# Kernel tuning notes

Measured on AMD Instinct MI355X. Metric: run time of the kernel, lower is better.

## Reference

```python
import jax, jax.numpy as jnp
import numpy as np

R = 50000          # residues
P = 24             # residue_pad_length
APR = 15           # atoms per residue (<= P)
N = R * APR        # total atoms
ACD = ATD = RCD = RID = 32
N_ATOM_CODES, N_ATOM_TYPES, N_RES_CODES, MAX_SEQ = 38, 6, 21, 1024
VEC_OUT, SC_OUT = 64, 256          # irreps_out = 64x1e + 256x0e
SC_IN = P * ACD + P * ATD + RCD + RID  # 1600 scalar inputs


def setup_inputs() -> dict:
    key = jax.random.key(0)
    ks = jax.random.split(key, 10)
    return {
        "residue_base_coords": jax.random.normal(ks[0], (R, 3), jnp.float32),
        "residue_relative_coords": jax.random.normal(ks[1], (N, 3), jnp.float32),
        "residue_code_index": jax.random.randint(ks[2], (R,), 0, N_RES_CODES),
        "residue_sequence_index": jnp.arange(R) % MAX_SEQ,
        "atom_code_index": jax.random.randint(ks[3], (N,), 0, N_ATOM_CODES),
        "atom_type_index": jax.random.randint(ks[4], (N,), 0, N_ATOM_TYPES),
        "residue_index_atomwise": jnp.repeat(jnp.arange(R), APR),  # sorted, APR atoms each
        "W_atom_code": jax.random.normal(ks[5], (N_ATOM_CODES, ACD), jnp.float32),
        "W_atom_type": jax.random.normal(ks[6], (N_ATOM_TYPES, ATD), jnp.float32),
        "W_res_code": jax.random.normal(ks[7], (N_RES_CODES, RCD), jnp.float32),
        "W_res_idx": jax.random.normal(ks[8], (MAX_SEQ, RID), jnp.float32),
        "W_vec": jax.random.normal(jax.random.fold_in(key, 1), (P, VEC_OUT), jnp.float32),
        "W_sc": jax.random.normal(ks[9], (SC_IN, SC_OUT), jnp.float32),
    }


def reference(residue_base_coords, residue_relative_coords, residue_code_index,
              residue_sequence_index, atom_code_index, atom_type_index,
              residue_index_atomwise, W_atom_code, W_atom_type, W_res_code,
              W_res_idx, W_vec, W_sc):
    R_ = residue_base_coords.shape[0]
    P_ = W_vec.shape[0]
    N_ = residue_index_atomwise.shape[0]
    ri = residue_index_atomwise
    # vectorized replacement of the per-residue python loop:
    # position of each atom within its residue (residue_index_atomwise is sorted)
    offsets = jnp.searchsorted(ri, jnp.arange(R_))            # first atom of each residue
    pos = jnp.arange(N_) - offsets[ri]                        # [N]
    # scatter atoms into padded [R, P, ...] layout (pad slots stay 0, like F.pad)
    mask = jnp.zeros((R_, P_), bool).at[ri, pos].set(True)
    rel = jnp.zeros((R_, P_, 3), residue_relative_coords.dtype).at[ri, pos].set(residue_relative_coords)
    codes = jnp.zeros((R_, P_), atom_code_index.dtype).at[ri, pos].set(atom_code_index)
    types = jnp.zeros((R_, P_), atom_type_index.dtype).at[ri, pos].set(atom_type_index)
    maskf = mask.astype(W_atom_code.dtype)[..., None]
    # embedding lookups, masked (pad embeddings zeroed as in the torch code)
    ac = (W_atom_code[codes] * maskf).reshape(R_, -1)         # [R, P*ACD]
    at = (W_atom_type[types] * maskf).reshape(R_, -1)         # [R, P*ATD]
    rc = W_res_code[residue_code_index]                       # [R, RCD]
    rix = W_res_idx[residue_sequence_index]                   # [R, RID]
    scalars = jnp.concatenate([ac, at, rc, rix], axis=-1)     # [R, SC_IN]
    # e3nn o3.Linear: l=1 channels mix only with l=1 (Px1e -> VEC_OUTx1e),
    # l=0 channels mix only with l=0; path-normalized by sqrt(fan_in), no bias.
    out_vec = jnp.einsum('rpc,pm->rmc', rel, W_vec) / jnp.sqrt(jnp.float32(P_))
    out_sc = (scalars @ W_sc) / jnp.sqrt(jnp.float32(scalars.shape[-1]))
    features = jnp.concatenate([out_vec.reshape(R_, -1), out_sc], axis=-1)  # [R, 3*VEC_OUT+SC_OUT]
    return residue_base_coords, features  # ResidueState(coords, features)
```

## Files before the change

kernel.cpp:

```cpp
#include <hip/hip_runtime.h>
#include <stdint.h>

static constexpr int P       = 24;
static constexpr int EMB_D   = 32;
static constexpr int N_AC    = 38;
static constexpr int N_AT    = 6;
static constexpr int N_RC    = 21;
static constexpr int MAXSEQ  = 1024;
static constexpr int VEC_OUT = 64;
static constexpr int SC_OUT  = 256;
static constexpr int FEAT    = 3 * VEC_OUT + SC_OUT;
static constexpr int CT      = N_AC * N_AT;
static constexpr int NROWS   = P * CT;
static constexpr int ROWB    = SC_OUT * 2;
static constexpr uint32_t ZROWB = (uint32_t)NROWS * ROWB;

__device__ __forceinline__ unsigned short f2bf(float f) {
    uint32_t x = __float_as_uint(f);
    uint32_t r = (x + 0x7FFFu + ((x >> 16) & 1u)) >> 16;
    return (unsigned short)r;
}

__global__ __launch_bounds__(256) void k1_init_build(
        const float* __restrict__ Wac, const float* __restrict__ Wat,
        const float* __restrict__ Wrc, const float* __restrict__ Wri,
        const float* __restrict__ Wsc,
        float* __restrict__ Ec, float* __restrict__ Et,
        float* __restrict__ Erc, float* __restrict__ Erix,
        int* __restrict__ starts, int* __restrict__ ends, int R) {
    int b = blockIdx.x;
    const int initB = (R + 255) / 256;
    if (b < initB) {
        int i = b * 256 + threadIdx.x;
        if (i < R) { starts[i] = 0; ends[i] = 0; }
        return;
    }
    b -= initB;
    const float* Wemb; float* E; int n_emb, sc_base, idx;
    if (b < P * N_AC) {
        Wemb = Wac; E = Ec; n_emb = N_AC; sc_base = 0; idx = b;
    } else if (b < P * N_AC + P * N_AT) {
        Wemb = Wat; E = Et; n_emb = N_AT; sc_base = P * EMB_D; idx = b - P * N_AC;
    } else if (b < P * N_AC + P * N_AT + N_RC) {
        Wemb = Wrc; E = Erc; n_emb = N_RC; sc_base = 2 * P * EMB_D;
        idx = b - (P * N_AC + P * N_AT);
    } else {
        Wemb = Wri; E = Erix; n_emb = MAXSEQ; sc_base = 2 * P * EMB_D + EMB_D;
        idx = b - (P * N_AC + P * N_AT + N_RC);
    }
    int p = idx / n_emb, e = idx % n_emb;
    int o = threadIdx.x;
    const float* wrow = Wemb + (size_t)e * EMB_D;
    const float* scol = Wsc + (size_t)(sc_base + p * EMB_D) * SC_OUT + o;
    float s = 0.f;
#pragma unroll
    for (int d = 0; d < EMB_D; ++d) s += wrow[d] * scol[(size_t)d * SC_OUT];
    E[(size_t)idx * SC_OUT + o] = s * 0.025f;
}

__global__ void k2_find_bounds(const int* __restrict__ ri, int* __restrict__ starts,
                               int* __restrict__ ends, int N) {
    int i = blockIdx.x * blockDim.x + threadIdx.x;
    if (i >= N) return;
    int r = ri[i];
    if (i == 0 || ri[i - 1] != r) starts[r] = i;
    if (i == N - 1 || ri[i + 1] != r) ends[r] = i + 1;
}

__global__ __launch_bounds__(256) void k3_fuse_prep(
        const float* __restrict__ Ec, const float* __restrict__ Et,
        unsigned short* __restrict__ Etab,
        const int* __restrict__ starts, const int* __restrict__ ends,
        const int* __restrict__ rcode, const int* __restrict__ rseq,
        const int* __restrict__ acode, const int* __restrict__ atype,
        const float* __restrict__ rel, const float* __restrict__ base,
        float* __restrict__ out_coords,
        int4* __restrict__ hdr, uint32_t* __restrict__ recArr, int R) {
    int b = blockIdx.x;
    if (b < NROWS + 1) {
        int o = threadIdx.x;
        if (b == NROWS) { Etab[(size_t)b * SC_OUT + o] = 0; return; }
        int j = b / CT, ct = b % CT, c = ct / N_AT, t = ct % N_AT;
        float s = Ec[((size_t)j * N_AC + c) * SC_OUT + o] +
                  Et[((size_t)j * N_AT + t) * SC_OUT + o];
        Etab[(size_t)b * SC_OUT + o] = f2bf(s);
        return;
    }
    b -= NROWS + 1;
    const int hdrB = (R + 255) >> 8;
    if (b < hdrB) {
        int i = b * 256 + threadIdx.x;
        if (i < R) {
            int st = starts[i];
            int c = ends[i] - st; if (c > P) c = P;
            hdr[i] = make_int4(st, c, rcode[i], rseq[i]);
        }
        return;
    }
    b -= hdrB;
    const int coordB = (3 * R + 1023) >> 10;
    if (b < coordB) {
        int i = b * 256 + threadIdx.x;
        int n4 = (3 * R) >> 2;
        if (i < n4)
            reinterpret_cast<float4*>(out_coords)[i] =
                reinterpret_cast<const float4*>(base)[i];
        if (i == n4) {
            for (int t = 4 * n4; t < 3 * R; ++t) out_coords[t] = base[t];
        }
        return;
    }
    b -= coordB;
    int i = b * 256 + threadIdx.x;
    if (i >= R * 64) return;
    int r = i >> 6, l = i & 63;
    int st = starts[r];
    int c = ends[r] - st; if (c > P) c = P;
    uint32_t out;
    if (l < 16) {
        out = ZROWB;
        if (l < c)
            out = (uint32_t)((l * CT + acode[st + l] * N_AT + atype[st + l]) * ROWB);
    } else {
        int idx = l - 16, k = idx / 3, cc = idx - k * 3;
        float v = 0.f;
        if (k < c) v = rel[(size_t)(st + k) * 3 + cc];
        out = __float_as_uint(v);
    }
    recArr[(size_t)r * 64 + l] = out;
}

__global__ __launch_bounds__(256, 4) void k4_residue(
        const int4* __restrict__ hdr, const uint32_t* __restrict__ recArr,
        const unsigned char* __restrict__ tab,
        const float* __restrict__ Erc, const float* __restrict__ Erix,
        const float* __restrict__ Wvec,
        const int* __restrict__ acode, const int* __restrict__ atype,
        const float* __restrict__ rel,
        float* __restrict__ out_feat, int R) {

    const int wave   = (blockIdx.x << 2) + (threadIdx.x >> 6);
    const int lane   = threadIdx.x & 63;
    const int lb     = lane * 8;
    const int lane4  = lane * 4;
    const int totalw = gridDim.x << 2;
    if (wave >= R) return;

    float w[16];
#pragma unroll
    for (int k = 0; k < 16; ++k) w[k] = Wvec[k * VEC_OUT + lane];

    uint32_t recA, recB;
    int4 hA, hB;
    float4 eaA, ebA, eaB, ebB;

    auto PRE = [&](uint32_t& rec, int4& h, float4& ea, float4& eb, int j) {
        int rr = __builtin_amdgcn_readfirstlane(j < R ? j : R - 1);
        h   = hdr[rr];
        rec = recArr[(size_t)rr * 64 + lane];
        ea  = *reinterpret_cast<const float4*>(Erc + (size_t)h.z * SC_OUT + lane4);
        eb  = *reinterpret_cast<const float4*>(Erix + (size_t)h.w * SC_OUT + lane4);
    };

    auto BODY = [&](uint32_t rec, const int4& h, const float4& ea, const float4& eb,
                    uint32_t& recN, int4& hN, float4& eaN, float4& ebN, int j) {
        uint2 g[16];
#pragma unroll
        for (int k = 0; k < 16; ++k) {
            uint32_t ro = (uint32_t)__builtin_amdgcn_readlane((int)rec, k);
            g[k] = *reinterpret_cast<const uint2*>(tab + ro + lb);
        }
        PRE(recN, hN, eaN, ebN, j + totalw);
        float a0 = ea.x + eb.x, a1 = ea.y + eb.y;
        float a2 = ea.z + eb.z, a3 = ea.w + eb.w;
        float v0 = 0.f, v1 = 0.f, v2 = 0.f;
#pragma unroll
        for (int k = 0; k < 16; ++k) {
            a0 += __uint_as_float(g[k].x << 16);
            a1 += __uint_as_float(g[k].x & 0xFFFF0000u);
            a2 += __uint_as_float(g[k].y << 16);
            a3 += __uint_as_float(g[k].y & 0xFFFF0000u);
            float sx = __uint_as_float((uint32_t)__builtin_amdgcn_readlane((int)rec, 16 + 3 * k));
            float sy = __uint_as_float((uint32_t)__builtin_amdgcn_readlane((int)rec, 17 + 3 * k));
            float sz = __uint_as_float((uint32_t)__builtin_amdgcn_readlane((int)rec, 18 + 3 * k));
            v0 = fmaf(sx, w[k], v0);
            v1 = fmaf(sy, w[k], v1);
            v2 = fmaf(sz, w[k], v2);
        }
        if (h.y > 16) {
            int st = h.x;
            for (int k = 16; k < h.y; ++k) {
                int c = acode[st + k], t = atype[st + k];
                uint32_t ro = (uint32_t)((k * CT + c * N_AT + t) * ROWB);
                uint2 gg = *reinterpret_cast<const uint2*>(tab + ro + lb);
                float ww = Wvec[k * VEC_OUT + lane];
                a0 += __uint_as_float(gg.x << 16);
                a1 += __uint_as_float(gg.x & 0xFFFF0000u);
                a2 += __uint_as_float(gg.y << 16);
                a3 += __uint_as_float(gg.y & 0xFFFF0000u);
                v0 = fmaf(rel[(size_t)(st + k) * 3], ww, v0);
                v1 = fmaf(rel[(size_t)(st + k) * 3 + 1], ww, v1);
                v2 = fmaf(rel[(size_t)(st + k) * 3 + 2], ww, v2);
            }
        }
        const float vs = 0.20412414523193150818f;
        float* frow = out_feat + (size_t)j * FEAT;
        frow[lane * 3 + 0] = v0 * vs;
        frow[lane * 3 + 1] = v1 * vs;
        frow[lane * 3 + 2] = v2 * vs;
        *reinterpret_cast<float4*>(frow + 3 * VEC_OUT + lane4) =
            make_float4(a0, a1, a2, a3);
    };

    PRE(recA, hA, eaA, ebA, wave);
    int j = wave;
    while (true) {
        BODY(recA, hA, eaA, ebA, recB, hB, eaB, ebB, j);
        j += totalw;
        if (j >= R) break;
        BODY(recB, hB, eaB, ebB, recA, hA, eaA, ebA, j);
        j += totalw;
        if (j >= R) break;
    }
}

extern "C" void kernel_launch(void* const* d_in, const int* in_sizes, int n_in,
                              void* d_out, int out_size, void* d_ws, size_t ws_size,
                              hipStream_t stream) {
    const float* base  = (const float*)d_in[0];
    const float* rel   = (const float*)d_in[1];
    const int*   rcode = (const int*)d_in[2];
    const int*   rseq  = (const int*)d_in[3];
    const int*   acode = (const int*)d_in[4];
    const int*   atype = (const int*)d_in[5];
    const int*   ri    = (const int*)d_in[6];
    const float* Wac   = (const float*)d_in[7];
    const float* Wat   = (const float*)d_in[8];
    const float* Wrc   = (const float*)d_in[9];
    const float* Wri   = (const float*)d_in[10];
    const float* Wv    = (const float*)d_in[11];
    const float* Wsc   = (const float*)d_in[12];

    const int R = in_sizes[0] / 3;
    const int N = in_sizes[6];

    float* out_coords = (float*)d_out;
    float* out_feat   = out_coords + (size_t)R * 3;

    char* ws = (char*)d_ws;
    size_t ofs = 0;
    auto alloc = [&](size_t bytes) {
        void* p = ws + ofs;
        ofs = (ofs + bytes + 255) & ~255ULL;
        return p;
    };
    int*            starts = (int*)alloc((size_t)R * 4);
    int*            ends   = (int*)alloc((size_t)R * 4);
    float*          Ec_f   = (float*)alloc((size_t)P * N_AC * SC_OUT * 4);
    float*          Et_f   = (float*)alloc((size_t)P * N_AT * SC_OUT * 4);
    float*          Erc_f  = (float*)alloc((size_t)N_RC * SC_OUT * 4);
    float*          Erix_f = (float*)alloc((size_t)MAXSEQ * SC_OUT * 4);
    unsigned short* Etab   = (unsigned short*)alloc((size_t)(NROWS + 1) * SC_OUT * 2);
    int4*           hdr    = (int4*)alloc((size_t)R * 16);
    uint32_t*       recArr = (uint32_t*)alloc((size_t)R * 64 * 4);
    (void)ws_size; (void)n_in; (void)out_size;

    const int initB  = (R + 255) / 256;
    const int k1B    = initB + P * N_AC + P * N_AT + N_RC + MAXSEQ;
    const int hdrB   = (R + 255) / 256;
    const int coordB = (3 * R + 1023) / 1024;
    const int recB   = (R * 64 + 255) / 256;
    const int k3B    = (NROWS + 1) + hdrB + coordB + recB;

    k1_init_build<<<k1B, 256, 0, stream>>>(Wac, Wat, Wrc, Wri, Wsc,
                                           Ec_f, Et_f, Erc_f, Erix_f, starts, ends, R);
    k2_find_bounds<<<(N + 255) / 256, 256, 0, stream>>>(ri, starts, ends, N);
    k3_fuse_prep<<<k3B, 256, 0, stream>>>(Ec_f, Et_f, Etab, starts, ends,
                                          rcode, rseq, acode, atype, rel, base,
                                          out_coords, hdr, recArr, R);
    k4_residue<<<1024, 256, 0, stream>>>(
        hdr, recArr, (const unsigned char*)Etab,
        Erc_f, Erix_f, Wv, acode, atype, rel, out_feat, R);
}
```

Before: 63.44 us.

## Store residue embedding tables in bf16 and software-pipeline gathers one residue ahead

The residue-code and sequence-index projection tables are now stored as bf16 instead of fp32, which halves their gather traffic and folds them into the same 18-entry gather array as the atom rows. The main kernel loop is restructured into a deeper software pipeline: record loads run two residues ahead and the table gathers one residue ahead, so the accumulation for one residue overlaps the memory latency of the next. The cost is higher register pressure from holding two 18-entry gather buffers, which could reduce occupancy, plus extra bf16 rounding on the residue embeddings.

```diff
diff --git a/kernel.cpp b/kernel.cpp
--- a/kernel.cpp
+++ b/kernel.cpp
@@ -26,7 +26,7 @@
         const float* __restrict__ Wrc, const float* __restrict__ Wri,
         const float* __restrict__ Wsc,
         float* __restrict__ Ec, float* __restrict__ Et,
-        float* __restrict__ Erc, float* __restrict__ Erix,
+        unsigned short* __restrict__ ErcH, unsigned short* __restrict__ ErixH,
         int* __restrict__ starts, int* __restrict__ ends, int R) {
     int b = blockIdx.x;
     const int initB = (R + 255) / 256;
@@ -36,17 +36,17 @@
         return;
     }
     b -= initB;
-    const float* Wemb; float* E; int n_emb, sc_base, idx;
+    const float* Wemb; int n_emb, sc_base, idx, sect;
     if (b < P * N_AC) {
-        Wemb = Wac; E = Ec; n_emb = N_AC; sc_base = 0; idx = b;
+        Wemb = Wac; n_emb = N_AC; sc_base = 0; idx = b; sect = 0;
     } else if (b < P * N_AC + P * N_AT) {
-        Wemb = Wat; E = Et; n_emb = N_AT; sc_base = P * EMB_D; idx = b - P * N_AC;
+        Wemb = Wat; n_emb = N_AT; sc_base = P * EMB_D; idx = b - P * N_AC; sect = 1;
     } else if (b < P * N_AC + P * N_AT + N_RC) {
-        Wemb = Wrc; E = Erc; n_emb = N_RC; sc_base = 2 * P * EMB_D;
-        idx = b - (P * N_AC + P * N_AT);
+        Wemb = Wrc; n_emb = N_RC; sc_base = 2 * P * EMB_D;
+        idx = b - (P * N_AC + P * N_AT); sect = 2;
     } else {
-        Wemb = Wri; E = Erix; n_emb = MAXSEQ; sc_base = 2 * P * EMB_D + EMB_D;
-        idx = b - (P * N_AC + P * N_AT + N_RC);
+        Wemb = Wri; n_emb = MAXSEQ; sc_base = 2 * P * EMB_D + EMB_D;
+        idx = b - (P * N_AC + P * N_AT + N_RC); sect = 3;
     }
     int p = idx / n_emb, e = idx % n_emb;
     int o = threadIdx.x;
@@ -55,7 +55,11 @@
     float s = 0.f;
 #pragma unroll
     for (int d = 0; d < EMB_D; ++d) s += wrow[d] * scol[(size_t)d * SC_OUT];
-    E[(size_t)idx * SC_OUT + o] = s * 0.025f;
+    s *= 0.025f;
+    if (sect == 0)      Ec[(size_t)idx * SC_OUT + o] = s;
+    else if (sect == 1) Et[(size_t)idx * SC_OUT + o] = s;
+    else if (sect == 2) ErcH[(size_t)idx * SC_OUT + o] = f2bf(s);
+    else                ErixH[(size_t)idx * SC_OUT + o] = f2bf(s);
 }
 
 __global__ void k2_find_bounds(const int* __restrict__ ri, int* __restrict__ starts,
@@ -133,7 +137,7 @@
 __global__ __launch_bounds__(256, 4) void k4_residue(
         const int4* __restrict__ hdr, const uint32_t* __restrict__ recArr,
         const unsigned char* __restrict__ tab,
-        const float* __restrict__ Erc, const float* __restrict__ Erix,
+        const unsigned char* __restrict__ ErcH, const unsigned char* __restrict__ ErixH,
         const float* __restrict__ Wvec,
         const int* __restrict__ acode, const int* __restrict__ atype,
         const float* __restrict__ rel,
@@ -142,7 +146,6 @@
     const int wave   = (blockIdx.x << 2) + (threadIdx.x >> 6);
     const int lane   = threadIdx.x & 63;
     const int lb     = lane * 8;
-    const int lane4  = lane * 4;
     const int totalw = gridDim.x << 2;
     if (wave >= R) return;
 
@@ -152,44 +155,50 @@
 
     uint32_t recA, recB;
     int4 hA, hB;
-    float4 eaA, ebA, eaB, ebB;
-
-    auto PRE = [&](uint32_t& rec, int4& h, float4& ea, float4& eb, int j) {
+    uint2 gA[18], gB[18];
+    float vxA, vyA, vzA, vxB, vyB, vzB;
+    int stA, cntA, stB, cntB;
+
+    auto REC = [&](uint32_t& rec, int4& h, int j) {
         int rr = __builtin_amdgcn_readfirstlane(j < R ? j : R - 1);
         h   = hdr[rr];
         rec = recArr[(size_t)rr * 64 + lane];
-        ea  = *reinterpret_cast<const float4*>(Erc + (size_t)h.z * SC_OUT + lane4);
-        eb  = *reinterpret_cast<const float4*>(Erix + (size_t)h.w * SC_OUT + lane4);
     };
 
-    auto BODY = [&](uint32_t rec, const int4& h, const float4& ea, const float4& eb,
-                    uint32_t& recN, int4& hN, float4& eaN, float4& ebN, int j) {
-        uint2 g[16];
+    auto GV = [&](uint2 (&g)[18], float& vx, float& vy, float& vz,
+                  int& st, int& cnt, uint32_t rec, const int4& h) {
 #pragma unroll
         for (int k = 0; k < 16; ++k) {
             uint32_t ro = (uint32_t)__builtin_amdgcn_readlane((int)rec, k);
             g[k] = *reinterpret_cast<const uint2*>(tab + ro + lb);
         }
-        PRE(recN, hN, eaN, ebN, j + totalw);
-        float a0 = ea.x + eb.x, a1 = ea.y + eb.y;
-        float a2 = ea.z + eb.z, a3 = ea.w + eb.w;
-        float v0 = 0.f, v1 = 0.f, v2 = 0.f;
+        g[16] = *reinterpret_cast<const uint2*>(ErcH + ((size_t)h.z << 9) + lb);
+        g[17] = *reinterpret_cast<const uint2*>(ErixH + ((size_t)h.w << 9) + lb);
+        vx = 0.f; vy = 0.f; vz = 0.f;
 #pragma unroll
         for (int k = 0; k < 16; ++k) {
+            float sx = __uint_as_float((uint32_t)__builtin_amdgcn_readlane((int)rec, 16 + 3 * k));
+            float sy = __uint_as_float((uint32_t)__builtin_amdgcn_readlane((int)rec, 17 + 3 * k));
+            float sz = __uint_as_float((uint32_t)__builtin_amdgcn_readlane((int)rec, 18 + 3 * k));
+            vx = fmaf(sx, w[k], vx);
+            vy = fmaf(sy, w[k], vy);
+            vz = fmaf(sz, w[k], vz);
+        }
+        st = h.x; cnt = h.y;
+    };
+
+    auto ACC = [&](const uint2 (&g)[18], float vx, float vy, float vz,
+                   int st, int cnt, int j) {
+        float a0 = 0.f, a1 = 0.f, a2 = 0.f, a3 = 0.f;
+#pragma unroll
+        for (int k = 0; k < 18; ++k) {
             a0 += __uint_as_float(g[k].x << 16);
             a1 += __uint_as_float(g[k].x & 0xFFFF0000u);
             a2 += __uint_as_float(g[k].y << 16);
             a3 += __uint_as_float(g[k].y & 0xFFFF0000u);
-            float sx = __uint_as_float((uint32_t)__builtin_amdgcn_readlane((int)rec, 16 + 3 * k));
-            float sy = __uint_as_float((uint32_t)__builtin_amdgcn_readlane((int)rec, 17 + 3 * k));
-            float sz = __uint_as_float((uint32_t)__builtin_amdgcn_readlane((int)rec, 18 + 3 * k));
-            v0 = fmaf(sx, w[k], v0);
-            v1 = fmaf(sy, w[k], v1);
-            v2 = fmaf(sz, w[k], v2);
-        }
-        if (h.y > 16) {
-            int st = h.x;
-            for (int k = 16; k < h.y; ++k) {
+        }
+        if (cnt > 16) {
+            for (int k = 16; k < cnt; ++k) {
                 int c = acode[st + k], t = atype[st + k];
                 uint32_t ro = (uint32_t)((k * CT + c * N_AT + t) * ROWB);
                 uint2 gg = *reinterpret_cast<const uint2*>(tab + ro + lb);
@@ -198,27 +207,34 @@
                 a1 += __uint_as_float(gg.x & 0xFFFF0000u);
                 a2 += __uint_as_float(gg.y << 16);
                 a3 += __uint_as_float(gg.y & 0xFFFF0000u);
-                v0 = fmaf(rel[(size_t)(st + k) * 3], ww, v0);
-                v1 = fmaf(rel[(size_t)(st + k) * 3 + 1], ww, v1);
-                v2 = fmaf(rel[(size_t)(st + k) * 3 + 2], ww, v2);
+                vx = fmaf(rel[(size_t)(st + k) * 3], ww, vx);
+                vy = fmaf(rel[(size_t)(st + k) * 3 + 1], ww, vy);
+                vz = fmaf(rel[(size_t)(st + k) * 3 + 2], ww, vz);
             }
         }
         const float vs = 0.20412414523193150818f;
         float* frow = out_feat + (size_t)j * FEAT;
-        frow[lane * 3 + 0] = v0 * vs;
-        frow[lane * 3 + 1] = v1 * vs;
-        frow[lane * 3 + 2] = v2 * vs;
-        *reinterpret_cast<float4*>(frow + 3 * VEC_OUT + lane4) =
+        frow[lane * 3 + 0] = vx * vs;
+        frow[lane * 3 + 1] = vy * vs;
+        frow[lane * 3 + 2] = vz * vs;
+        *reinterpret_cast<float4*>(frow + 3 * VEC_OUT + lane * 4) =
             make_float4(a0, a1, a2, a3);
     };
 
-    PRE(recA, hA, eaA, ebA, wave);
     int j = wave;
+    REC(recA, hA, j);
+    REC(recB, hB, j + totalw);
+    GV(gB, vxB, vyB, vzB, stB, cntB, recA, hA);
+
     while (true) {
-        BODY(recA, hA, eaA, ebA, recB, hB, eaB, ebB, j);
+        REC(recA, hA, j + 2 * totalw);
+        GV(gA, vxA, vyA, vzA, stA, cntA, recB, hB);
+        ACC(gB, vxB, vyB, vzB, stB, cntB, j);
         j += totalw;
         if (j >= R) break;
-        BODY(recB, hB, eaB, ebB, recA, hA, eaA, ebA, j);
+        REC(recB, hB, j + 2 * totalw);
+        GV(gB, vxB, vyB, vzB, stB, cntB, recA, hA);
+        ACC(gA, vxA, vyA, vzA, stA, cntA, j);
         j += totalw;
         if (j >= R) break;
     }
@@ -258,8 +274,8 @@
     int*            ends   = (int*)alloc((size_t)R * 4);
     float*          Ec_f   = (float*)alloc((size_t)P * N_AC * SC_OUT * 4);
     float*          Et_f   = (float*)alloc((size_t)P * N_AT * SC_OUT * 4);
-    float*          Erc_f  = (float*)alloc((size_t)N_RC * SC_OUT * 4);
-    float*          Erix_f = (float*)alloc((size_t)MAXSEQ * SC_OUT * 4);
+    unsigned short* ErcH   = (unsigned short*)alloc((size_t)N_RC * SC_OUT * 2);
+    unsigned short* ErixH  = (unsigned short*)alloc((size_t)MAXSEQ * SC_OUT * 2);
     unsigned short* Etab   = (unsigned short*)alloc((size_t)(NROWS + 1) * SC_OUT * 2);
     int4*           hdr    = (int4*)alloc((size_t)R * 16);
     uint32_t*       recArr = (uint32_t*)alloc((size_t)R * 64 * 4);
@@ -273,12 +289,13 @@
     const int k3B    = (NROWS + 1) + hdrB + coordB + recB;
 
     k1_init_build<<<k1B, 256, 0, stream>>>(Wac, Wat, Wrc, Wri, Wsc,
-                                           Ec_f, Et_f, Erc_f, Erix_f, starts, ends, R);
+                                           Ec_f, Et_f, ErcH, ErixH, starts, ends, R);
     k2_find_bounds<<<(N + 255) / 256, 256, 0, stream>>>(ri, starts, ends, N);
     k3_fuse_prep<<<k3B, 256, 0, stream>>>(Ec_f, Et_f, Etab, starts, ends,
                                           rcode, rseq, acode, atype, rel, base,
                                           out_coords, hdr, recArr, R);
     k4_residue<<<1024, 256, 0, stream>>>(
         hdr, recArr, (const unsigned char*)Etab,
-        Erc_f, Erix_f, Wv, acode, atype, rel, out_feat, R);
-}
+        (const unsigned char*)ErcH, (const unsigned char*)ErixH,
+        Wv, acode, atype, rel, out_feat, R);
+}
```

New measurement: 85.94 us. 1.35x slower.
